# Kernel optimization log

Hardware: AMD Instinct MI355X
Metric: run time of the kernel (lower is better)

## Reference

```python
import jax, jax.numpy as jnp
import numpy as np

NUM_HEADS = 12

def setup_inputs() -> dict:
    key = jax.random.key(0)
    k1, k2, k3 = jax.random.split(key, 3)
    B, N, C = 8, 2048, 768
    x = jax.random.normal(k1, (B, N, C), dtype=jnp.float32)
    w_qkv = jax.random.normal(k2, (3 * C, C), dtype=jnp.float32) * (C ** -0.5)
    w_proj = jax.random.normal(k3, (C, C), dtype=jnp.float32) * (C ** -0.5)
    b_proj = jnp.zeros((C,), dtype=jnp.float32)
    return {"x": x, "w_qkv": w_qkv, "w_proj": w_proj, "b_proj": b_proj}

def reference(x, w_qkv, w_proj, b_proj):
    B, N, C = x.shape
    H = NUM_HEADS
    D = C // H
    scale = D ** -0.5
    # qkv: [B,N,3C] -> [3,B,H,N,D]
    qkv = (x @ w_qkv.T).reshape(B, N, 3, H, D).transpose(2, 0, 3, 1, 4)
    q, k, v = qkv[0], qkv[1], qkv[2]
    attn = jnp.einsum('bhnd,bhmd->bhnm', q, k) * scale  # [B,H,N,N]
    attn = jax.nn.softmax(attn, axis=-1)
    out = jnp.einsum('bhnm,bhmd->bhnd', attn, v)  # [B,H,N,D]
    out = out.transpose(0, 2, 1, 3).reshape(B, N, C)
    return out @ w_proj.T + b_proj
```

## Files before the change

### kernel.cpp

```cpp
#include <hip/hip_runtime.h>

typedef __bf16 bf16;
typedef __attribute__((ext_vector_type(8))) __bf16 bf16x8;
typedef __attribute__((ext_vector_type(4))) __bf16 bf16x4;
typedef __attribute__((ext_vector_type(4))) float f32x4;

#define NBATCH 8
#define NHEAD  12
#define SEQ    2048
#define DH     64
#define CDIM   768
#define MROWS  (NBATCH*SEQ)
#define NQKV   (3*CDIM)

__device__ __forceinline__ f32x4 mfma16(bf16x8 a, bf16x8 b, f32x4 c) {
  return __builtin_amdgcn_mfma_f32_16x16x32_bf16(a, b, c, 0, 0, 0);
}

__device__ __forceinline__ void gload_lds16(const void* g, void* l) {
  __builtin_amdgcn_global_load_lds((const __attribute__((address_space(1))) void*)g,
                                   (__attribute__((address_space(3))) void*)l,
                                   16, 0, 0);
}

__device__ __forceinline__ unsigned cvt_pk_bf16(float lo, float hi) {
  unsigned r;
  asm("v_cvt_pk_bf16_f32 %0, %1, %2" : "=v"(r) : "v"(lo), "v"(hi));
  return r;
}

__device__ __forceinline__ float exp2_raw(float x) {
  float r;
  asm("v_exp_f32 %0, %1" : "=v"(r) : "v"(x));
  return r;
}

__global__ void cvt_bf16(const float* __restrict__ src, bf16* __restrict__ dst, int n8) {
  int i = blockIdx.x * 256 + threadIdx.x;
  if (i >= n8) return;
  const float4* s4 = (const float4*)src;
  float4 a = s4[2*i], c = s4[2*i+1];
  bf16x8 o;
  o[0]=(bf16)a.x; o[1]=(bf16)a.y; o[2]=(bf16)a.z; o[3]=(bf16)a.w;
  o[4]=(bf16)c.x; o[5]=(bf16)c.y; o[6]=(bf16)c.z; o[7]=(bf16)c.w;
  *(bf16x8*)(dst + (size_t)i*8) = o;
}

template <int OUT_F32>
__global__ __launch_bounds__(256, 2)
void gemm_bt(const bf16* __restrict__ A, const bf16* __restrict__ Bm,
             void* __restrict__ Cout, const float* __restrict__ bias,
             int M, int Nn, int K) {
  __shared__ bf16 As[128*32];
  __shared__ bf16 Bs[128*32];
  const int tid = threadIdx.x, wid = tid >> 6, lane = tid & 63;
  const int g = lane >> 4, ln = lane & 15;
  const int ntn = Nn >> 7;
  const int gsz = 32 * ntn;
  const int grp = blockIdx.x / gsz;
  const int rem = blockIdx.x - grp * gsz;
  const int tm = grp * 32 + (rem & 31);
  const int tn = rem >> 5;
  const int m0 = tm << 7, n0 = tn << 7;
  const int wr = wid >> 1, wc = wid & 1;

  const int srow = lane >> 2;
  const int sslot = lane & 3;

  f32x4 acc[4][4] = {};

  const int nkt = K >> 5;
  for (int kt = 0; kt < nkt; ++kt) {
    if (kt) __syncthreads();
    #pragma unroll
    for (int i = 0; i < 2; ++i) {
      int c = wid * 2 + i;
      int row = c * 16 + srow;
      int colA = kt * 32 + ((sslot ^ (row & 3)) << 3);
      gload_lds16(A + (size_t)(m0 + row) * K + colA, &As[c * 512]);
      gload_lds16(Bm + (size_t)(n0 + row) * K + colA, &Bs[c * 512]);
    }
    __syncthreads();

    bf16x8 aF[4], bF[4];
    #pragma unroll
    for (int m = 0; m < 4; ++m) {
      int row = wr * 64 + m * 16 + ln;
      aF[m] = *(const bf16x8*)&As[row * 32 + ((g ^ (row & 3)) << 3)];
    }
    #pragma unroll
    for (int n = 0; n < 4; ++n) {
      int row = wc * 64 + n * 16 + ln;
      bF[n] = *(const bf16x8*)&Bs[row * 32 + ((g ^ (row & 3)) << 3)];
    }
    #pragma unroll
    for (int m = 0; m < 4; ++m)
      #pragma unroll
      for (int n = 0; n < 4; ++n)
        acc[m][n] = mfma16(aF[m], bF[n], acc[m][n]);
  }

  #pragma unroll
  for (int m = 0; m < 4; ++m) {
    int rowb = m0 + wr * 64 + m * 16 + g * 4;
    #pragma unroll
    for (int n = 0; n < 4; ++n) {
      int col = n0 + wc * 64 + n * 16 + ln;
      float bv = OUT_F32 ? bias[col] : 0.f;
      #pragma unroll
      for (int r = 0; r < 4; ++r) {
        if (OUT_F32)
          ((float*)Cout)[(size_t)(rowb + r) * Nn + col] = acc[m][n][r] + bv;
        else
          ((bf16*)Cout)[(size_t)(rowb + r) * Nn + col] = (bf16)acc[m][n][r];
      }
    }
  }
}

__global__ __launch_bounds__(256)
void split_v(const bf16* __restrict__ qkv, bf16* __restrict__ Vt) {
  __shared__ bf16 vlds[64 * 72];
  const int nt = blockIdx.x, bh = blockIdx.y;
  const int b = bh / NHEAD, h = bh % NHEAD;
  const int tid = threadIdx.x;
  const int nl = tid >> 2, quad = tid & 3;

  const bf16* s = qkv + ((size_t)(b * SEQ + nt * 64 + nl)) * NQKV + 2 * CDIM + h * DH + quad * 16;
  *(bf16x8*)&vlds[nl * 72 + quad * 16] = *(const bf16x8*)s;
  *(bf16x8*)&vlds[nl * 72 + quad * 16 + 8] = *(const bf16x8*)(s + 8);
  __syncthreads();
  const int dl = tid >> 2;
  bf16x8 w0, w1;
  #pragma unroll
  for (int j = 0; j < 8; ++j) {
    w0[j] = vlds[(quad * 16 + j) * 72 + dl];
    w1[j] = vlds[(quad * 16 + 8 + j) * 72 + dl];
  }
  bf16* d = Vt + ((size_t)bh * DH + dl) * SEQ + nt * 64 + quad * 16;
  *(bf16x8*)d = w0;
  *(bf16x8*)(d + 8) = w1;
}

__global__ __launch_bounds__(128, 2)
void attn_fwd9(const bf16* __restrict__ qkv, const bf16* __restrict__ Vt,
               bf16* __restrict__ Oa) {
  __shared__ bf16 Ks[2][64 * 64];
  __shared__ bf16 Vs[2][64 * 64];
  const int tid = threadIdx.x, wid = tid >> 6, lane = tid & 63;
  const int g = lane >> 4, ln = lane & 15;
  const int qt = blockIdx.x, bh = blockIdx.y;
  const int b = bh / NHEAD, h = bh % NHEAD;

  const bf16* QrowA = qkv + ((size_t)b * SEQ + qt * 64 + wid * 32 + ln) * NQKV + h * DH;
  const bf16* QrowB = QrowA + (size_t)16 * NQKV;
  const bf16x8 qA0 = *(const bf16x8*)(QrowA + g * 8);
  const bf16x8 qA1 = *(const bf16x8*)(QrowA + 32 + g * 8);
  const bf16x8 qB0 = *(const bf16x8*)(QrowB + g * 8);
  const bf16x8 qB1 = *(const bf16x8*)(QrowB + 32 + g * 8);

  const int sr = lane >> 3, sl = lane & 7;
  const bf16* kp[4];
  const bf16* vp[4];
  int lofs[4];
  #pragma unroll
  for (int i = 0; i < 4; ++i) {
    const int c = wid * 4 + i;
    const int pr = c * 8 + sr;
    const int sw = (sl ^ (pr & 7)) << 3;
    const int keyK = ((pr >> 5) & 1) * 32 + ((pr >> 4) & 1) * 4 + ((pr >> 2) & 3) * 8 + (pr & 3);
    kp[i] = qkv + ((size_t)b * SEQ + keyK) * NQKV + CDIM + h * DH + sw;
    vp[i] = Vt + ((size_t)bh * DH + pr) * SEQ + sw;
    lofs[i] = c * 512;
  }
  const size_t KADV = (size_t)64 * NQKV;

  const int e7 = ln & 7;
  const int off0 = ln * 64 + ((g ^ e7) << 3);
  const int off1 = ln * 64 + (((4 | g) ^ e7) << 3);

  const bf16 one = (bf16)1.0f;
  const bf16x8 onesF = {one, one, one, one, one, one, one, one};

  f32x4 oA[4] = {}, oB[4] = {};
  f32x4 laccA = {0.f, 0.f, 0.f, 0.f}, laccB = {0.f, 0.f, 0.f, 0.f};
  float mA = -3.0e38f, mB = -3.0e38f;
  const float SC = 0.125f * 1.44269504088896f;

  #pragma unroll
  for (int i = 0; i < 4; ++i) {
    gload_lds16(kp[i], &Ks[0][lofs[i]]);
    gload_lds16(vp[i], &Vs[0][lofs[i]]);
    kp[i] += KADV; vp[i] += 64;
  }
  #pragma unroll
  for (int i = 0; i < 4; ++i) {
    gload_lds16(kp[i], &Ks[1][lofs[i]]);
    gload_lds16(vp[i], &Vs[1][lofs[i]]);
    kp[i] += KADV; vp[i] += 64;
  }

  const int NT = SEQ / 64;
  for (int t = 0; t < NT; ++t) {
    if (t == NT - 1) asm volatile("s_waitcnt vmcnt(0)" ::: "memory");
    else             asm volatile("s_waitcnt vmcnt(8)" ::: "memory");
    __builtin_amdgcn_s_barrier();
    __builtin_amdgcn_sched_barrier(0);

    const bf16* KsB = &Ks[t & 1][0];
    const bf16* VsB = &Vs[t & 1][0];

    f32x4 sA[4] = {}, sB[4] = {};
    #pragma unroll
    for (int nt = 0; nt < 4; ++nt) {
      bf16x8 kF0 = *(const bf16x8*)(KsB + off0 + nt * 1024);
      bf16x8 kF1 = *(const bf16x8*)(KsB + off1 + nt * 1024);
      sA[nt] = mfma16(kF0, qA0, sA[nt]);
      sA[nt] = mfma16(kF1, qA1, sA[nt]);
      sB[nt] = mfma16(kF0, qB0, sB[nt]);
      sB[nt] = mfma16(kF1, qB1, sB[nt]);
    }

    float a0 = fmaxf(fmaxf(sA[0][0], sA[0][1]), fmaxf(sA[0][2], sA[0][3]));
    float a1 = fmaxf(fmaxf(sA[1][0], sA[1][1]), fmaxf(sA[1][2], sA[1][3]));
    float a2 = fmaxf(fmaxf(sA[2][0], sA[2][1]), fmaxf(sA[2][2], sA[2][3]));
    float a3 = fmaxf(fmaxf(sA[3][0], sA[3][1]), fmaxf(sA[3][2], sA[3][3]));
    float rA = fmaxf(fmaxf(a0, a1), fmaxf(a2, a3));
    rA = fmaxf(rA, __shfl_xor(rA, 16, 64));
    rA = fmaxf(rA, __shfl_xor(rA, 32, 64));
    float b0 = fmaxf(fmaxf(sB[0][0], sB[0][1]), fmaxf(sB[0][2], sB[0][3]));
    float b1 = fmaxf(fmaxf(sB[1][0], sB[1][1]), fmaxf(sB[1][2], sB[1][3]));
    float b2 = fmaxf(fmaxf(sB[2][0], sB[2][1]), fmaxf(sB[2][2], sB[2][3]));
    float b3 = fmaxf(fmaxf(sB[3][0], sB[3][1]), fmaxf(sB[3][2], sB[3][3]));
    float rB = fmaxf(fmaxf(b0, b1), fmaxf(b2, b3));
    rB = fmaxf(rB, __shfl_xor(rB, 16, 64));
    rB = fmaxf(rB, __shfl_xor(rB, 32, 64));
    const float rsA = rA * SC, rsB = rB * SC;

    if (__any(rsA > mA + 8.0f || rsB > mB + 8.0f)) {
      float nmA = fmaxf(mA, rsA), nmB = fmaxf(mB, rsB);
      float alA = exp2_raw(mA - nmA), alB = exp2_raw(mB - nmB);
      mA = nmA; mB = nmB;
      float alrA[4], alrB[4];
      #pragma unroll
      for (int r = 0; r < 4; ++r) {
        alrA[r] = __shfl(alA, g * 4 + r, 64);
        alrB[r] = __shfl(alB, g * 4 + r, 64);
      }
      #pragma unroll
      for (int dt = 0; dt < 4; ++dt)
        #pragma unroll
        for (int r = 0; r < 4; ++r) { oA[dt][r] *= alrA[r]; oB[dt][r] *= alrB[r]; }
      #pragma unroll
      for (int r = 0; r < 4; ++r) { laccA[r] *= alrA[r]; laccB[r] *= alrB[r]; }
    }

    bf16x8 pA[2], pB[2];
    #pragma unroll
    for (int kk = 0; kk < 2; ++kk) {
      union { bf16x8 v; unsigned u[4]; } w;
      w.u[0] = cvt_pk_bf16(exp2_raw(fmaf(sA[2*kk][0], SC, -mA)),
                           exp2_raw(fmaf(sA[2*kk][1], SC, -mA)));
      w.u[1] = cvt_pk_bf16(exp2_raw(fmaf(sA[2*kk][2], SC, -mA)),
                           exp2_raw(fmaf(sA[2*kk][3], SC, -mA)));
      w.u[2] = cvt_pk_bf16(exp2_raw(fmaf(sA[2*kk+1][0], SC, -mA)),
                           exp2_raw(fmaf(sA[2*kk+1][1], SC, -mA)));
      w.u[3] = cvt_pk_bf16(exp2_raw(fmaf(sA[2*kk+1][2], SC, -mA)),
                           exp2_raw(fmaf(sA[2*kk+1][3], SC, -mA)));
      pA[kk] = w.v;
      w.u[0] = cvt_pk_bf16(exp2_raw(fmaf(sB[2*kk][0], SC, -mB)),
                           exp2_raw(fmaf(sB[2*kk][1], SC, -mB)));
      w.u[1] = cvt_pk_bf16(exp2_raw(fmaf(sB[2*kk][2], SC, -mB)),
                           exp2_raw(fmaf(sB[2*kk][3], SC, -mB)));
      w.u[2] = cvt_pk_bf16(exp2_raw(fmaf(sB[2*kk+1][0], SC, -mB)),
                           exp2_raw(fmaf(sB[2*kk+1][1], SC, -mB)));
      w.u[3] = cvt_pk_bf16(exp2_raw(fmaf(sB[2*kk+1][2], SC, -mB)),
                           exp2_raw(fmaf(sB[2*kk+1][3], SC, -mB)));
      pB[kk] = w.v;
    }

    #pragma unroll
    for (int kk = 0; kk < 2; ++kk) {
      laccA = mfma16(pA[kk], onesF, laccA);
      laccB = mfma16(pB[kk], onesF, laccB);
      const int voff = kk ? off1 : off0;
      #pragma unroll
      for (int dt = 0; dt < 4; ++dt) {
        bf16x8 vF = *(const bf16x8*)(VsB + voff + dt * 1024);
        oA[dt] = mfma16(pA[kk], vF, oA[dt]);
        oB[dt] = mfma16(pB[kk], vF, oB[dt]);
      }
    }

    __builtin_amdgcn_sched_barrier(0);
    __builtin_amdgcn_s_barrier();
    if (t + 2 < NT) {
      #pragma unroll
      for (int i = 0; i < 4; ++i) {
        gload_lds16(kp[i], &Ks[t & 1][lofs[i]]);
        gload_lds16(vp[i], &Vs[t & 1][lofs[i]]);
        kp[i] += KADV; vp[i] += 64;
      }
    }
  }

  float invA[4], invB[4];
  #pragma unroll
  for (int r = 0; r < 4; ++r) { invA[r] = 1.0f / laccA[r]; invB[r] = 1.0f / laccB[r]; }

  #pragma unroll
  for (int r = 0; r < 4; ++r) {
    bf16* OrA = Oa + ((size_t)b * SEQ + qt * 64 + wid * 32 + g * 4 + r) * CDIM + h * DH + ln;
    bf16* OrB = OrA + (size_t)16 * CDIM;
    #pragma unroll
    for (int dt = 0; dt < 4; ++dt) {
      OrA[dt * 16] = (bf16)(oA[dt][r] * invA[r]);
      OrB[dt * 16] = (bf16)(oB[dt][r] * invB[r]);
    }
  }
}

extern "C" void kernel_launch(void* const* d_in, const int* in_sizes, int n_in,
                              void* d_out, int out_size, void* d_ws, size_t ws_size,
                              hipStream_t stream) {
  const float* x      = (const float*)d_in[0];
  const float* w_qkv  = (const float*)d_in[1];
  const float* w_proj = (const float*)d_in[2];
  const float* b_proj = (const float*)d_in[3];

  char* ws = (char*)d_ws;
  bf16* x_bf    = (bf16*)(ws + 0);
  bf16* wqkv_bf = (bf16*)(ws + 25165824);
  bf16* wproj_bf= (bf16*)(ws + 28704768);
  bf16* qkv     = (bf16*)(ws + 29884416);
  bf16* attn_o  = (bf16*)(ws + 105381888);
  bf16* Vtb     = (bf16*)(ws + 130547712);

  cvt_bf16<<<dim3((MROWS*CDIM/8 + 255)/256), 256, 0, stream>>>(x, x_bf, MROWS*CDIM/8);
  cvt_bf16<<<dim3((NQKV*CDIM/8 + 255)/256), 256, 0, stream>>>(w_qkv, wqkv_bf, NQKV*CDIM/8);
  cvt_bf16<<<dim3((CDIM*CDIM/8 + 255)/256), 256, 0, stream>>>(w_proj, wproj_bf, CDIM*CDIM/8);

  gemm_bt<0><<<dim3((MROWS/128)*(NQKV/128)), 256, 0, stream>>>(
      x_bf, wqkv_bf, qkv, nullptr, MROWS, NQKV, CDIM);

  split_v<<<dim3(SEQ/64, NBATCH*NHEAD), 256, 0, stream>>>(qkv, Vtb);

  attn_fwd9<<<dim3(SEQ/64, NBATCH*NHEAD), 128, 0, stream>>>(qkv, Vtb, attn_o);

  gemm_bt<1><<<dim3((MROWS/128)*(CDIM/128)), 256, 0, stream>>>(
      attn_o, wproj_bf, (float*)d_out, b_proj, MROWS, CDIM, CDIM);
}
```

Measured before the change: 308.7 us.

## Enlarge attention block to 256 query rows across 8 waves sharing K/V tiles

The attention kernel now runs 8 waves per block covering 256 query rows instead of 2 waves covering 64. Each K/V tile staged in LDS is shared by four times as many queries, so global K/V traffic per query drops. Each wave now issues one K and one V async load per tile, and the waitcnt threshold is adjusted to match. The cost is fewer blocks (768 instead of 3072), a larger barrier group per tile, and a heavier occupancy requirement set by launch bounds of 512 threads with a minimum of 6 blocks.

```diff
diff --git a/kernel.cpp b/kernel.cpp
--- a/kernel.cpp
+++ b/kernel.cpp
@@ -142,17 +142,17 @@
   *(bf16x8*)(d + 8) = w1;
 }
 
-__global__ __launch_bounds__(128, 2)
-void attn_fwd9(const bf16* __restrict__ qkv, const bf16* __restrict__ Vt,
-               bf16* __restrict__ Oa) {
-  __shared__ bf16 Ks[2][64 * 64];
-  __shared__ bf16 Vs[2][64 * 64];
+__global__ __launch_bounds__(512, 6)
+void attn_fwd11(const bf16* __restrict__ qkv, const bf16* __restrict__ Vt,
+                bf16* __restrict__ Oa) {
+  __shared__ bf16 Ks[2][4096];
+  __shared__ bf16 Vs[2][4096];
   const int tid = threadIdx.x, wid = tid >> 6, lane = tid & 63;
   const int g = lane >> 4, ln = lane & 15;
   const int qt = blockIdx.x, bh = blockIdx.y;
   const int b = bh / NHEAD, h = bh % NHEAD;
 
-  const bf16* QrowA = qkv + ((size_t)b * SEQ + qt * 64 + wid * 32 + ln) * NQKV + h * DH;
+  const bf16* QrowA = qkv + ((size_t)b * SEQ + qt * 256 + wid * 32 + ln) * NQKV + h * DH;
   const bf16* QrowB = QrowA + (size_t)16 * NQKV;
   const bf16x8 qA0 = *(const bf16x8*)(QrowA + g * 8);
   const bf16x8 qA1 = *(const bf16x8*)(QrowA + 32 + g * 8);
@@ -160,19 +160,12 @@
   const bf16x8 qB1 = *(const bf16x8*)(QrowB + 32 + g * 8);
 
   const int sr = lane >> 3, sl = lane & 7;
-  const bf16* kp[4];
-  const bf16* vp[4];
-  int lofs[4];
-  #pragma unroll
-  for (int i = 0; i < 4; ++i) {
-    const int c = wid * 4 + i;
-    const int pr = c * 8 + sr;
-    const int sw = (sl ^ (pr & 7)) << 3;
-    const int keyK = ((pr >> 5) & 1) * 32 + ((pr >> 4) & 1) * 4 + ((pr >> 2) & 3) * 8 + (pr & 3);
-    kp[i] = qkv + ((size_t)b * SEQ + keyK) * NQKV + CDIM + h * DH + sw;
-    vp[i] = Vt + ((size_t)bh * DH + pr) * SEQ + sw;
-    lofs[i] = c * 512;
-  }
+  const int pr = wid * 8 + sr;
+  const int sw = (sl ^ (pr & 7)) << 3;
+  const int keyK = ((pr >> 5) & 1) * 32 + ((pr >> 4) & 1) * 4 + ((pr >> 2) & 3) * 8 + (pr & 3);
+  const bf16* kp = qkv + ((size_t)b * SEQ + keyK) * NQKV + CDIM + h * DH + sw;
+  const bf16* vp = Vt + ((size_t)bh * DH + pr) * SEQ + sw;
+  const int lofs = wid * 512;
   const size_t KADV = (size_t)64 * NQKV;
 
   const int e7 = ln & 7;
@@ -187,23 +180,17 @@
   float mA = -3.0e38f, mB = -3.0e38f;
   const float SC = 0.125f * 1.44269504088896f;
 
-  #pragma unroll
-  for (int i = 0; i < 4; ++i) {
-    gload_lds16(kp[i], &Ks[0][lofs[i]]);
-    gload_lds16(vp[i], &Vs[0][lofs[i]]);
-    kp[i] += KADV; vp[i] += 64;
-  }
-  #pragma unroll
-  for (int i = 0; i < 4; ++i) {
-    gload_lds16(kp[i], &Ks[1][lofs[i]]);
-    gload_lds16(vp[i], &Vs[1][lofs[i]]);
-    kp[i] += KADV; vp[i] += 64;
-  }
+  gload_lds16(kp, &Ks[0][lofs]);
+  gload_lds16(vp, &Vs[0][lofs]);
+  kp += KADV; vp += 64;
+  gload_lds16(kp, &Ks[1][lofs]);
+  gload_lds16(vp, &Vs[1][lofs]);
+  kp += KADV; vp += 64;
 
   const int NT = SEQ / 64;
   for (int t = 0; t < NT; ++t) {
     if (t == NT - 1) asm volatile("s_waitcnt vmcnt(0)" ::: "memory");
-    else             asm volatile("s_waitcnt vmcnt(8)" ::: "memory");
+    else             asm volatile("s_waitcnt vmcnt(2)" ::: "memory");
     __builtin_amdgcn_s_barrier();
     __builtin_amdgcn_sched_barrier(0);
 
@@ -295,12 +282,9 @@
     __builtin_amdgcn_sched_barrier(0);
     __builtin_amdgcn_s_barrier();
     if (t + 2 < NT) {
-      #pragma unroll
-      for (int i = 0; i < 4; ++i) {
-        gload_lds16(kp[i], &Ks[t & 1][lofs[i]]);
-        gload_lds16(vp[i], &Vs[t & 1][lofs[i]]);
-        kp[i] += KADV; vp[i] += 64;
-      }
+      gload_lds16(kp, &Ks[t & 1][lofs]);
+      gload_lds16(vp, &Vs[t & 1][lofs]);
+      kp += KADV; vp += 64;
     }
   }
 
@@ -310,7 +294,7 @@
 
   #pragma unroll
   for (int r = 0; r < 4; ++r) {
-    bf16* OrA = Oa + ((size_t)b * SEQ + qt * 64 + wid * 32 + g * 4 + r) * CDIM + h * DH + ln;
+    bf16* OrA = Oa + ((size_t)b * SEQ + qt * 256 + wid * 32 + g * 4 + r) * CDIM + h * DH + ln;
     bf16* OrB = OrA + (size_t)16 * CDIM;
     #pragma unroll
     for (int dt = 0; dt < 4; ++dt) {
@@ -345,7 +329,7 @@
 
   split_v<<<dim3(SEQ/64, NBATCH*NHEAD), 256, 0, stream>>>(qkv, Vtb);
 
-  attn_fwd9<<<dim3(SEQ/64, NBATCH*NHEAD), 128, 0, stream>>>(qkv, Vtb, attn_o);
+  attn_fwd11<<<dim3(SEQ/256, NBATCH*NHEAD), 512, 0, stream>>>(qkv, Vtb, attn_o);
 
   gemm_bt<1><<<dim3((MROWS/128)*(CDIM/128)), 256, 0, stream>>>(
       attn_o, wproj_bf, (float*)d_out, b_proj, MROWS, CDIM, CDIM);
```

Measured after the change: 796.9 us. 2.58x slower.
